# Kernel optimization log

Hardware: AMD Instinct MI355X
Metric: run time of the kernel (lower is better)

## Reference

```python
import jax, jax.numpy as jnp
import numpy as np

BETA1 = 0.9
BETA2 = 0.8
THRESH = 1.0  # snntorch Leaky default threshold

T, B, NI, NH, NO = 100, 1024, 256, 512, 10


def setup_inputs() -> dict:
    key = jax.random.key(0)
    kx, k1, k2 = jax.random.split(key, 3)
    x = jax.random.normal(kx, (T, B, NI), dtype=jnp.float32)
    # Weight_synapse 'bin_random_prob' init: binary {0, w} with given probs
    W1 = (jax.random.uniform(k1, (NH, NI)) < 0.8).astype(jnp.float32) * 0.5
    W2 = (jax.random.uniform(k2, (NO, NH)) < 0.5).astype(jnp.float32) * 0.5
    return {"x": x, "W1": W1, "W2": W2}


def _lif(mem, cur, beta):
    # snntorch Leaky, reset_mechanism='subtract': reset from previous mem,
    # then mem = beta*mem + cur - reset*threshold; spk = heaviside(mem - thr)
    reset = (mem > THRESH).astype(cur.dtype)
    mem = beta * mem + cur - reset * THRESH
    spk = (mem > THRESH).astype(cur.dtype)
    return spk, mem


def reference(x, W1, W2):
    b = x.shape[1]
    mem1_0 = jnp.zeros((b, W1.shape[0]), x.dtype)
    mem2_0 = jnp.zeros((b, W2.shape[0]), x.dtype)

    def step(carry, xt):
        mem1, mem2 = carry
        cur1 = xt @ W1.T                      # [B, NH]
        spk1, mem1 = _lif(mem1, cur1, BETA1)
        cur2 = spk1 @ W2.T                    # [B, NO]
        spk2, mem2 = _lif(mem2, cur2, BETA2)
        return (mem1, mem2), (cur1, cur2, spk1, spk2, mem1, mem2)

    _, (cur1, cur2, spk1, spk2, mem1, mem2) = jax.lax.scan(step, (mem1_0, mem2_0), x)
    # matches {'cur':[c1,c2],'spks':[s1,s2],'mem':[m1,m2]}, each stacked on time
    return cur1, cur2, spk1, spk2, mem1, mem2
```

## Files before the change

### kernel.cpp

```cpp
#include <hip/hip_runtime.h>

#define TT 100
#define BB 1024
#define NI 256
#define NH 512
#define NO 10
#define TB (TT*BB)
#define GK 512
#define GN 512

constexpr long long C1_OFF = 0;
constexpr long long C2_OFF = 52428800LL;
constexpr long long S1_OFF = 53452800LL;
constexpr long long S2_OFF = 105881600LL;
constexpr long long M1_OFF = 106905600LL;
constexpr long long M2_OFF = 159334400LL;

typedef short bf16x8 __attribute__((ext_vector_type(8)));
typedef float f32x4 __attribute__((ext_vector_type(4)));

__device__ __forceinline__ unsigned int rne_bf16(float f) {
    unsigned int u = __float_as_uint(f);
    return (u + 0x7fffu + ((u >> 16) & 1u)) >> 16;
}

__device__ __forceinline__ unsigned int pack_hilo(float f) {
    unsigned int hi = rne_bf16(f);
    float hif = __uint_as_float(hi << 16);
    float e = f - hif;
    unsigned int lo = rne_bf16(e);
    return (hi & 0xffffu) | (lo << 16);
}

__device__ __forceinline__ void pack4(uint4& d, const float4& a) {
    d.x = pack_hilo(a.x); d.y = pack_hilo(a.y); d.z = pack_hilo(a.z); d.w = pack_hilo(a.w);
}

__device__ __forceinline__ void barrier_lds() {
    asm volatile("s_waitcnt lgkmcnt(0)" ::: "memory");
    __builtin_amdgcn_s_barrier();
}

__global__ void prep_w_kernel(const float* __restrict__ W1, short* __restrict__ Wp) {
    int i = blockIdx.x * blockDim.x + threadIdx.x;
    if (i >= NH * NI / 4) return;
    float4 v = ((const float4*)W1)[i];
    float f[4] = {v.x, v.y, v.z, v.w};
    uint4 o;
    unsigned int* op = &o.x;
    #pragma unroll
    for (int j = 0; j < 4; ++j) {
        unsigned int hb = __float_as_uint(f[j]) >> 16;
        op[j] = hb | (hb << 16);
    }
    ((uint4*)Wp)[i] = o;
}

__launch_bounds__(256, 3)
__global__ void gemm1_kernel(const float* __restrict__ x, const short* __restrict__ Wp,
                             float* __restrict__ C) {
    __shared__ short As[2][128][40];
    const int tid = threadIdx.x;
    const int bid = blockIdx.x;
    const int x8 = bid & 7;
    const int g8 = bid >> 3;
    const int p  = g8 & 3;
    const int panel = (g8 >> 2) * 8 + x8;
    const int m0 = (799 - panel) * 128;
    const int n0 = p * 128;
    const int wid = tid >> 6;
    const int lane = tid & 63;
    const int wm = (wid >> 1) * 64;
    const int wn = (wid & 1) * 64;

    f32x4 acc[4][4] = {};

    const int srow = tid >> 2;
    const int sc4 = tid & 3;
    const long long ax0 = (long long)(m0 + srow) * NI + sc4 * 4;
    const long long ax1 = ax0 + 64LL * NI;

    const int fr = lane & 15;
    const int fk = (lane >> 4) * 8;
    const int g  = lane >> 4;

    const short* wrow0 = Wp + (long long)(n0 + wn + fr) * GK + g * 8;

    bf16x8 wreg[2][4];
    #pragma unroll
    for (int i = 0; i < 4; ++i)
        wreg[0][i] = *(const bf16x8*)(wrow0 + (long long)i * 16 * GK);

    uint4 pa0, pa1;
    {
        float4 t0a = *(const float4*)&x[ax0];
        float4 t0b = *(const float4*)&x[ax1];
        uint4 q0, q1;
        pack4(q0, t0a); pack4(q1, t0b);
        *(uint4*)&As[0][srow][sc4 * 8]      = q0;
        *(uint4*)&As[0][srow + 64][sc4 * 8] = q1;
        float4 t1a = *(const float4*)&x[ax0 + 16];
        float4 t1b = *(const float4*)&x[ax1 + 16];
        pack4(pa0, t1a); pack4(pa1, t1b);
    }
    float4 raw0a = *(const float4*)&x[ax0 + 32];
    float4 raw0b = *(const float4*)&x[ax1 + 32];
    float4 raw1a = *(const float4*)&x[ax0 + 48];
    float4 raw1b = *(const float4*)&x[ax1 + 48];
    barrier_lds();

    #pragma unroll
    for (int kt = 0; kt < 16; ++kt) {
        const int cur = kt & 1;
        const int nxt = cur ^ 1;

        if (kt + 1 < 16) {
            #pragma unroll
            for (int i = 0; i < 4; ++i)
                wreg[nxt][i] = *(const bf16x8*)(wrow0 + (long long)i * 16 * GK + (kt + 1) * 32);
            *(uint4*)&As[nxt][srow][sc4 * 8]      = pa0;
            *(uint4*)&As[nxt][srow + 64][sc4 * 8] = pa1;
        }
        if (kt + 2 < 16) {
            if (cur == 0) { pack4(pa0, raw0a); pack4(pa1, raw0b); }
            else          { pack4(pa0, raw1a); pack4(pa1, raw1b); }
        }
        if (kt + 4 < 16) {
            if (cur == 0) {
                raw0a = *(const float4*)&x[ax0 + (long long)(kt + 4) * 16];
                raw0b = *(const float4*)&x[ax1 + (long long)(kt + 4) * 16];
            } else {
                raw1a = *(const float4*)&x[ax0 + (long long)(kt + 4) * 16];
                raw1b = *(const float4*)&x[ax1 + (long long)(kt + 4) * 16];
            }
        }

        bf16x8 af[4];
        #pragma unroll
        for (int i = 0; i < 4; ++i)
            af[i] = *(const bf16x8*)&As[cur][wm + i * 16 + fr][fk];
        #pragma unroll
        for (int i = 0; i < 4; ++i)
            #pragma unroll
            for (int j = 0; j < 4; ++j)
                acc[i][j] = __builtin_amdgcn_mfma_f32_16x16x32_bf16(af[i], wreg[cur][j], acc[i][j], 0, 0, 0);

        if (kt + 1 < 16) barrier_lds();
    }

    const int col = lane & 15;
    const int rbase = (lane >> 4) * 4;
    #pragma unroll
    for (int i = 0; i < 4; ++i) {
        #pragma unroll
        for (int j = 0; j < 4; ++j) {
            long long base = (long long)(m0 + wm + i * 16 + rbase) * GN + (n0 + wn + j * 16 + col);
            #pragma unroll
            for (int r = 0; r < 4; ++r)
                C[base + (long long)r * GN] = acc[i][j][r];
        }
    }
}

__launch_bounds__(512)
__global__ void lif_kernel(const float* __restrict__ cur1, const float* __restrict__ W2,
                           float* __restrict__ out) {
    const int b = blockIdx.x;
    const int h = threadIdx.x;
    const int w = h >> 6;
    const int lane = h & 63;

    __shared__ unsigned long long wmks[2][2][8];
    __shared__ unsigned long long w2ms[NO][8];

    #pragma unroll
    for (int o = 0; o < NO; ++o) {
        unsigned long long mk = __ballot(W2[o * NH + h] != 0.0f);
        if (lane == 0) w2ms[o][w] = mk;
    }
    __syncthreads();
    unsigned long long w2m[8];
    if (h < NO) {
        #pragma unroll
        for (int i = 0; i < 8; ++i) w2m[i] = w2ms[h][i];
    }

    float m1 = 0.0f, m2 = 0.0f;
    const long long idx1 = (long long)b * NH + h;
    const float* c1p = cur1 + idx1;
    float* s1p = out + S1_OFF + idx1;
    float* m1p = out + M1_OFF + idx1;
    const long long st1 = (long long)BB * NH;

    float c1a = c1p[0];
    float c1b = c1p[st1];
    for (int t = 0; t < TT; t += 2) {
        const int par = (t >> 1) & 1;

        float c1c = 0.0f, c1d = 0.0f;
        if (t + 2 < TT) c1c = c1p[(long long)(t + 2) * st1];
        if (t + 3 < TT) c1d = c1p[(long long)(t + 3) * st1];

        float rst = (m1 > 1.0f) ? 1.0f : 0.0f;
        m1 = 0.9f * m1 + c1a - rst;
        float s1a = (m1 > 1.0f) ? 1.0f : 0.0f;
        s1p[(long long)t * st1] = s1a;
        m1p[(long long)t * st1] = m1;
        unsigned long long mka = __ballot(s1a != 0.0f);
        if (lane == 0) wmks[par][0][w] = mka;

        float rstb = (m1 > 1.0f) ? 1.0f : 0.0f;
        m1 = 0.9f * m1 + c1b - rstb;
        float s1b = (m1 > 1.0f) ? 1.0f : 0.0f;
        s1p[(long long)(t + 1) * st1] = s1b;
        m1p[(long long)(t + 1) * st1] = m1;
        unsigned long long mkb = __ballot(s1b != 0.0f);
        if (lane == 0) wmks[par][1][w] = mkb;

        barrier_lds();

        if (h < NO) {
            #pragma unroll
            for (int j = 0; j < 2; ++j) {
                int cnt = 0;
                #pragma unroll
                for (int i = 0; i < 8; ++i) cnt += __popcll(wmks[par][j][i] & w2m[i]);
                float c2 = 0.5f * (float)cnt;
                float rst2 = (m2 > 1.0f) ? 1.0f : 0.0f;
                m2 = 0.8f * m2 + c2 - rst2;
                float s2 = (m2 > 1.0f) ? 1.0f : 0.0f;
                long long o2 = (long long)(t + j) * (BB * NO) + b * NO + h;
                out[C2_OFF + o2] = c2;
                out[S2_OFF + o2] = s2;
                out[M2_OFF + o2] = m2;
            }
        }
        c1a = c1c; c1b = c1d;
    }
}

extern "C" void kernel_launch(void* const* d_in, const int* in_sizes, int n_in,
                              void* d_out, int out_size, void* d_ws, size_t ws_size,
                              hipStream_t stream) {
    const float* x  = (const float*)d_in[0];
    const float* W1 = (const float*)d_in[1];
    const float* W2 = (const float*)d_in[2];
    float* out = (float*)d_out;

    short* Wp = (short*)(out + S1_OFF);
    float* C1 = out + C1_OFF;

    prep_w_kernel<<<(NH * NI / 4 + 255) / 256, 256, 0, stream>>>(W1, Wp);
    gemm1_kernel<<<(TB / 128) * (GN / 128), 256, 0, stream>>>(x, Wp, C1);
    lif_kernel<<<BB, NH, 0, stream>>>(C1, W2, out);
}
```

Measured before the change: 294.7 us.

## Stage half-K x tiles in LDS and pre-swizzle W1 into fragment-order image

The x tile is now loaded in two half-K chunks of 128 columns into a single large LDS buffer, with one barrier per half instead of one per k-step. The old version ran a register-prefetch double-buffered pipeline. The weight prep kernel writes W1 in MFMA fragment order, so each lane reads one contiguous 16-byte chunk per fragment instead of strided rows. This removes per-iteration barriers and makes weight loads coalesced. The cost is a larger LDS footprint, occupancy lowered to 2 blocks, and x loads that no longer overlap the MFMAs within each half.

```diff
diff --git a/kernel.cpp b/kernel.cpp
--- a/kernel.cpp
+++ b/kernel.cpp
@@ -36,30 +36,35 @@
     d.x = pack_hilo(a.x); d.y = pack_hilo(a.y); d.z = pack_hilo(a.z); d.w = pack_hilo(a.w);
 }
 
+__device__ __forceinline__ unsigned int dup_w(float f) {
+    unsigned int hb = __float_as_uint(f) >> 16;
+    return hb | (hb << 16);
+}
+
 __device__ __forceinline__ void barrier_lds() {
     asm volatile("s_waitcnt lgkmcnt(0)" ::: "memory");
     __builtin_amdgcn_s_barrier();
 }
 
-__global__ void prep_w_kernel(const float* __restrict__ W1, short* __restrict__ Wp) {
+__global__ void prep_w_kernel(const float* __restrict__ W1, short* __restrict__ Wimg) {
     int i = blockIdx.x * blockDim.x + threadIdx.x;
-    if (i >= NH * NI / 4) return;
-    float4 v = ((const float4*)W1)[i];
-    float f[4] = {v.x, v.y, v.z, v.w};
+    if (i >= 4 * 16 * 8 * 64) return;
+    int l  = i & 63;
+    int rb = (i >> 6) & 7;
+    int kt = (i >> 9) & 15;
+    int p  = i >> 13;
+    int row = p * 128 + rb * 16 + (l & 15);
+    int kb  = kt * 16 + (l >> 4) * 4;
+    float4 w = *(const float4*)&W1[(long long)row * NI + kb];
     uint4 o;
-    unsigned int* op = &o.x;
-    #pragma unroll
-    for (int j = 0; j < 4; ++j) {
-        unsigned int hb = __float_as_uint(f[j]) >> 16;
-        op[j] = hb | (hb << 16);
-    }
-    ((uint4*)Wp)[i] = o;
-}
-
-__launch_bounds__(256, 3)
-__global__ void gemm1_kernel(const float* __restrict__ x, const short* __restrict__ Wp,
+    o.x = dup_w(w.x); o.y = dup_w(w.y); o.z = dup_w(w.z); o.w = dup_w(w.w);
+    ((uint4*)Wimg)[i] = o;
+}
+
+__launch_bounds__(256, 2)
+__global__ void gemm1_kernel(const float* __restrict__ x, const short* __restrict__ Wimg,
                              float* __restrict__ C) {
-    __shared__ short As[2][128][40];
+    __shared__ short As[128][264];
     const int tid = threadIdx.x;
     const int bid = blockIdx.x;
     const int x8 = bid & 7;
@@ -75,77 +80,51 @@
 
     f32x4 acc[4][4] = {};
 
-    const int srow = tid >> 2;
-    const int sc4 = tid & 3;
-    const long long ax0 = (long long)(m0 + srow) * NI + sc4 * 4;
-    const long long ax1 = ax0 + 64LL * NI;
-
     const int fr = lane & 15;
     const int fk = (lane >> 4) * 8;
-    const int g  = lane >> 4;
-
-    const short* wrow0 = Wp + (long long)(n0 + wn + fr) * GK + g * 8;
+    const int rb0 = wn >> 4;
+
+    const short* wbase = Wimg + (long long)p * 65536;
 
     bf16x8 wreg[2][4];
     #pragma unroll
-    for (int i = 0; i < 4; ++i)
-        wreg[0][i] = *(const bf16x8*)(wrow0 + (long long)i * 16 * GK);
-
-    uint4 pa0, pa1;
-    {
-        float4 t0a = *(const float4*)&x[ax0];
-        float4 t0b = *(const float4*)&x[ax1];
-        uint4 q0, q1;
-        pack4(q0, t0a); pack4(q1, t0b);
-        *(uint4*)&As[0][srow][sc4 * 8]      = q0;
-        *(uint4*)&As[0][srow + 64][sc4 * 8] = q1;
-        float4 t1a = *(const float4*)&x[ax0 + 16];
-        float4 t1b = *(const float4*)&x[ax1 + 16];
-        pack4(pa0, t1a); pack4(pa1, t1b);
-    }
-    float4 raw0a = *(const float4*)&x[ax0 + 32];
-    float4 raw0b = *(const float4*)&x[ax1 + 32];
-    float4 raw1a = *(const float4*)&x[ax0 + 48];
-    float4 raw1b = *(const float4*)&x[ax1 + 48];
-    barrier_lds();
-
-    #pragma unroll
-    for (int kt = 0; kt < 16; ++kt) {
-        const int cur = kt & 1;
-        const int nxt = cur ^ 1;
-
-        if (kt + 1 < 16) {
+    for (int j = 0; j < 4; ++j)
+        wreg[0][j] = *(const bf16x8*)(wbase + (0 * 8 + rb0 + j) * 512 + lane * 8);
+
+    #pragma unroll
+    for (int half = 0; half < 2; ++half) {
+        #pragma unroll
+        for (int it = 0; it < 16; ++it) {
+            int idx = it * 256 + tid;
+            int row = idx >> 5, c4 = idx & 31;
+            float4 a = *(const float4*)&x[(long long)(m0 + row) * NI + half * 128 + c4 * 4];
+            uint4 pa; pack4(pa, a);
+            *(uint4*)&As[row][c4 * 8] = pa;
+        }
+        barrier_lds();
+
+        #pragma unroll
+        for (int ktl = 0; ktl < 8; ++ktl) {
+            const int ktg = half * 8 + ktl;
+            const int cur = ktg & 1, nxt = cur ^ 1;
+
+            if (ktg + 1 < 16) {
+                #pragma unroll
+                for (int j = 0; j < 4; ++j)
+                    wreg[nxt][j] = *(const bf16x8*)(wbase + ((ktg + 1) * 8 + rb0 + j) * 512 + lane * 8);
+            }
+
+            bf16x8 af[4];
             #pragma unroll
             for (int i = 0; i < 4; ++i)
-                wreg[nxt][i] = *(const bf16x8*)(wrow0 + (long long)i * 16 * GK + (kt + 1) * 32);
-            *(uint4*)&As[nxt][srow][sc4 * 8]      = pa0;
-            *(uint4*)&As[nxt][srow + 64][sc4 * 8] = pa1;
-        }
-        if (kt + 2 < 16) {
-            if (cur == 0) { pack4(pa0, raw0a); pack4(pa1, raw0b); }
-            else          { pack4(pa0, raw1a); pack4(pa1, raw1b); }
-        }
-        if (kt + 4 < 16) {
-            if (cur == 0) {
-                raw0a = *(const float4*)&x[ax0 + (long long)(kt + 4) * 16];
-                raw0b = *(const float4*)&x[ax1 + (long long)(kt + 4) * 16];
-            } else {
-                raw1a = *(const float4*)&x[ax0 + (long long)(kt + 4) * 16];
-                raw1b = *(const float4*)&x[ax1 + (long long)(kt + 4) * 16];
-            }
-        }
-
-        bf16x8 af[4];
-        #pragma unroll
-        for (int i = 0; i < 4; ++i)
-            af[i] = *(const bf16x8*)&As[cur][wm + i * 16 + fr][fk];
-        #pragma unroll
-        for (int i = 0; i < 4; ++i)
-            #pragma unroll
-            for (int j = 0; j < 4; ++j)
-                acc[i][j] = __builtin_amdgcn_mfma_f32_16x16x32_bf16(af[i], wreg[cur][j], acc[i][j], 0, 0, 0);
-
-        if (kt + 1 < 16) barrier_lds();
+                af[i] = *(const bf16x8*)&As[wm + i * 16 + fr][ktl * 32 + fk];
+            #pragma unroll
+            for (int i = 0; i < 4; ++i)
+                #pragma unroll
+                for (int j = 0; j < 4; ++j)
+                    acc[i][j] = __builtin_amdgcn_mfma_f32_16x16x32_bf16(af[i], wreg[cur][j], acc[i][j], 0, 0, 0);
+        }
+        if (half == 0) barrier_lds();
     }
 
     const int col = lane & 15;
@@ -250,7 +229,7 @@
     short* Wp = (short*)(out + S1_OFF);
     float* C1 = out + C1_OFF;
 
-    prep_w_kernel<<<(NH * NI / 4 + 255) / 256, 256, 0, stream>>>(W1, Wp);
+    prep_w_kernel<<<(4 * 16 * 8 * 64 + 255) / 256, 256, 0, stream>>>(W1, Wp);
     gemm1_kernel<<<(TB / 128) * (GN / 128), 256, 0, stream>>>(x, Wp, C1);
     lif_kernel<<<BB, NH, 0, stream>>>(C1, W2, out);
 }
```

Result: faster. 288.0 us (-2.3%).
